# Performance work log

Hardware: AMD Instinct MI355X
Metric: run time of the kernel (lower is better)

The kernel has to match this reference:

```python
import jax, jax.numpy as jnp
import numpy as np

N_NODES = 100000
N_EDGES = 1600000


def gcn_conv(x, src, dst, W, b, n_nodes):
    # PyG GCNConv: h = x @ W; symmetric normalization with self-loops; scatter-add; + bias
    deg = jax.ops.segment_sum(jnp.ones_like(src, dtype=x.dtype), dst, num_segments=n_nodes)
    dinv = jax.lax.rsqrt(jnp.where(deg > 0, deg, 1.0))
    norm = dinv[src] * dinv[dst]              # [E+N]
    h = x @ W                                  # [N, out]
    msg = h[src] * norm[:, None]               # gather + scale (irregular access)
    out = jax.ops.segment_sum(msg, dst, num_segments=n_nodes)  # scatter-add aggregate
    return out + b


def setup_inputs() -> dict:
    key = jax.random.key(0)
    k1, k2, k3, k4 = jax.random.split(key, 4)
    x = jax.random.normal(k1, (N_NODES, 128), dtype=jnp.float32)
    edge_index = jax.random.randint(k2, (2, N_EDGES), 0, N_NODES, dtype=jnp.int64)
    W1 = jax.random.normal(k3, (128, 48), dtype=jnp.float32) * (1.0 / np.sqrt(128))
    b1 = jnp.zeros((48,), dtype=jnp.float32)
    W2 = jax.random.normal(k4, (48, 16), dtype=jnp.float32) * (1.0 / np.sqrt(48))
    b2 = jnp.zeros((16,), dtype=jnp.float32)
    return {"x": x, "edge_index": edge_index, "W1": W1, "b1": b1, "W2": W2, "b2": b2}


def reference(x, edge_index, W1, b1, W2, b2):
    n = x.shape[0]
    loops = jnp.arange(n, dtype=edge_index.dtype)
    src = jnp.concatenate([edge_index[0], loops])  # add self-loops
    dst = jnp.concatenate([edge_index[1], loops])
    h = gcn_conv(x, src, dst, W1, b1, n)
    h = jax.nn.relu(h)
    h = gcn_conv(h, src, dst, W2, b2, n)
    h = jax.nn.relu(h)
    return jax.nn.softmax(h, axis=1)
```

## Files before the change

### kernel.cpp

```cpp
#include <hip/hip_runtime.h>
#include <hip/hip_bf16.h>
#include <hip/hip_fp16.h>


#define TILE 4096

typedef _Float16 half8 __attribute__((ext_vector_type(8)));
typedef float floatx4 __attribute__((ext_vector_type(4)));

__global__ __launch_bounds__(256) void k_bhist(const int* __restrict__ dst, int E,
                                               int* __restrict__ Hw, int nbuck) {
    __shared__ int h[512];
    int t = threadIdx.x;
    for (int i = t; i < nbuck; i += 256) h[i] = 0;
    __syncthreads();
    int base = blockIdx.x * TILE;
#pragma unroll
    for (int r = 0; r < TILE / 256; ++r) {
        int e = base + r * 256 + t;
        if (e < E) atomicAdd(&h[dst[e] >> 8], 1);
    }
    __syncthreads();
    for (int i = t; i < nbuck; i += 256) Hw[blockIdx.x * nbuck + i] = h[i];
}

__global__ __launch_bounds__(256) void k_bsum(const int* __restrict__ Hw, int nTiles,
                                              int nbuck, int* __restrict__ btot) {
    int wid = (blockIdx.x * 256 + threadIdx.x) >> 6;
    int lane = threadIdx.x & 63;
    if (wid >= nbuck) return;
    int sum = 0;
    for (int tt = lane; tt < nTiles; tt += 64) sum += Hw[tt * nbuck + wid];
#pragma unroll
    for (int off = 32; off; off >>= 1) sum += __shfl_down(sum, off);
    if (lane == 0) btot[wid] = sum;
}

__global__ __launch_bounds__(512) void k_bscan2(const int* __restrict__ btot, int nbuck,
                                                int* __restrict__ bstart) {
    __shared__ int s[512];
    int t = threadIdx.x;
    int v = (t < nbuck) ? btot[t] : 0;
    s[t] = v;
    __syncthreads();
    for (int off = 1; off < 512; off <<= 1) {
        int tmp = (t >= off) ? s[t - off] : 0;
        __syncthreads();
        s[t] += tmp;
        __syncthreads();
    }
    if (t < nbuck) bstart[t] = s[t] - v;
    if (t == nbuck - 1) bstart[nbuck] = s[t];
}

__global__ __launch_bounds__(256) void k_boff(int* __restrict__ Hw, int nTiles,
                                              int nbuck, const int* __restrict__ bstart) {
    int wid = (blockIdx.x * 256 + threadIdx.x) >> 6;
    int lane = threadIdx.x & 63;
    if (wid >= nbuck) return;
    int running = bstart[wid];
    for (int chunk = 0; chunk < nTiles; chunk += 64) {
        int tt = chunk + lane;
        int v = (tt < nTiles) ? Hw[tt * nbuck + wid] : 0;
        int incl = v;
#pragma unroll
        for (int off = 1; off < 64; off <<= 1) {
            int u = __shfl_up(incl, off);
            if (lane >= off) incl += u;
        }
        if (tt < nTiles) Hw[tt * nbuck + wid] = running + (incl - v);
        running += __shfl(incl, 63);
    }
}

__global__ __launch_bounds__(256) void k_bscatter(const int* __restrict__ ei, int E,
                                                  const int* __restrict__ Hw, int nbuck,
                                                  int* __restrict__ ebuf) {
    __shared__ int cur[512];
    int t = threadIdx.x;
    for (int i = t; i < nbuck; i += 256) cur[i] = Hw[blockIdx.x * nbuck + i];
    __syncthreads();
    int base = blockIdx.x * TILE;
#pragma unroll
    for (int r = 0; r < TILE / 256; ++r) {
        int e = base + r * 256 + t;
        if (e < E) {
            int s = ei[e];
            int d = ei[E + e];
            int pos = atomicAdd(&cur[d >> 8], 1);
            ebuf[pos] = s | ((d & 255) << 17);
        }
    }
}

__global__ __launch_bounds__(256) void k_csrfill(const int* __restrict__ ebuf,
                                                 const int* __restrict__ bstart,
                                                 int* __restrict__ csr,
                                                 int* __restrict__ rowstart,
                                                 float* __restrict__ dinv, int N) {
    __shared__ int lcnt[256];
    __shared__ int lscan[256];
    __shared__ int lcur[256];
    int t = threadIdx.x;
    int nodebase = blockIdx.x << 8;
    int segs = bstart[blockIdx.x];
    int sege = bstart[blockIdx.x + 1];
    lcnt[t] = 0;
    __syncthreads();
    for (int i = segs + t; i < sege; i += 256)
        atomicAdd(&lcnt[((unsigned)ebuf[i]) >> 17], 1);
    __syncthreads();
    int v = lcnt[t];
    lscan[t] = v;
    __syncthreads();
    for (int off = 1; off < 256; off <<= 1) {
        int tmp = (t >= off) ? lscan[t - off] : 0;
        __syncthreads();
        lscan[t] += tmp;
        __syncthreads();
    }
    int excl = lscan[t] - v;
    int node = nodebase + t;
    int rs = segs + excl;
    if (node < N) {
        rowstart[node] = rs;
        dinv[node] = rsqrtf((float)(v + 1));
        if (node == N - 1) rowstart[N] = rs + v;
    }
    lcur[t] = rs;
    __syncthreads();
    for (int i = segs + t; i < sege; i += 256) {
        int pk = ebuf[i];
        int pos = atomicAdd(&lcur[((unsigned)pk) >> 17], 1);
        csr[pos] = pk & 0x1FFFF;
    }
}

__global__ __launch_bounds__(256) void k_gemm1(const float* __restrict__ x,
                                               const float* __restrict__ W1,
                                               const float* __restrict__ dinv,
                                               __half* __restrict__ h1p, int N) {
    __shared__ _Float16 wt[48 * 136];
    int t = threadIdx.x;
    for (int i = t; i < 128 * 48; i += 256) {
        int k = i / 48, c = i % 48;
        wt[c * 136 + k] = (_Float16)W1[i];
    }
    __syncthreads();

    int wave = t >> 6, lane = t & 63;
    int g = lane >> 4;
    int rtile = blockIdx.x * 64 + wave * 16;
    int rowA = rtile + (lane & 15);
    const float* xrow = x + (size_t)(rowA < N ? rowA : N - 1) * 128;
    int c0 = lane & 15;

    floatx4 acc[3];
#pragma unroll
    for (int nt = 0; nt < 3; ++nt)
#pragma unroll
        for (int q = 0; q < 4; ++q) acc[nt][q] = 0.f;

#pragma unroll
    for (int kc = 0; kc < 4; ++kc) {
        int k0 = kc * 32 + g * 8;
        float4 a0 = *(const float4*)(xrow + k0);
        float4 a1 = *(const float4*)(xrow + k0 + 4);
        half8 a;
        a[0] = (_Float16)a0.x; a[1] = (_Float16)a0.y;
        a[2] = (_Float16)a0.z; a[3] = (_Float16)a0.w;
        a[4] = (_Float16)a1.x; a[5] = (_Float16)a1.y;
        a[6] = (_Float16)a1.z; a[7] = (_Float16)a1.w;
#pragma unroll
        for (int nt = 0; nt < 3; ++nt) {
            half8 b = *(const half8*)(&wt[(nt * 16 + c0) * 136 + k0]);
            acc[nt] = __builtin_amdgcn_mfma_f32_16x16x32_f16(a, b, acc[nt], 0, 0, 0);
        }
    }

    int rbase = rtile + g * 4;
#pragma unroll
    for (int j = 0; j < 4; ++j) {
        int r = rbase + j;
        if (r < N) {
            float dr = dinv[r];
#pragma unroll
            for (int nt = 0; nt < 3; ++nt)
                h1p[(size_t)r * 48 + nt * 16 + c0] = __float2half(acc[nt][j] * dr);
        }
    }
}

__global__ __launch_bounds__(256) void k_agg1(const __half* __restrict__ h1p,
                                              const int* __restrict__ csr,
                                              const int* __restrict__ rowstart,
                                              const float* __restrict__ dinv,
                                              const float* __restrict__ b1,
                                              __half* __restrict__ r1h, int N) {
    int wave = threadIdx.x >> 6;
    int lane = threadIdx.x & 63;
    int v = blockIdx.x * 4 + wave;
    if (v >= N) return;
    int grp = lane >> 3;
    int sub = lane & 7;

    int start = rowstart[v];
    int d = rowstart[v + 1] - start;
    float dv = dinv[v];
    const int* cs = csr + start;
    const char* h1b = (const char*)h1p;

    float acc[8] = {0.f, 0.f, 0.f, 0.f, 0.f, 0.f, 0.f, 0.f};

    for (int base = 0; base < d; base += 64) {
        int sreg = (base + lane < d) ? cs[base + lane] : 0;
        int nb = min(64, d - base);
        for (int j = 0; j < 8 && j * 8 < nb; ++j) {
            int s = __shfl(sreg, j * 8 + grp);
            if (j * 8 + grp < nb && sub < 6) {
                float4 rv = *(const float4*)(h1b + (size_t)s * 96 + sub * 16);
                const __half2* hp = (const __half2*)&rv;
#pragma unroll
                for (int q = 0; q < 4; ++q) {
                    float2 f = __half22float2(hp[q]);
                    acc[q * 2] += f.x;
                    acc[q * 2 + 1] += f.y;
                }
            }
        }
    }
#pragma unroll
    for (int i = 0; i < 8; ++i) {
        acc[i] += __shfl_xor(acc[i], 8);
        acc[i] += __shfl_xor(acc[i], 16);
        acc[i] += __shfl_xor(acc[i], 32);
    }
    if (grp == 0 && sub < 6) {
        float4 sv = *(const float4*)(h1b + (size_t)v * 96 + sub * 16);
        const __half2* hp = (const __half2*)&sv;
        __half2 ob[4];
#pragma unroll
        for (int q = 0; q < 4; ++q) {
            float2 sf = __half22float2(hp[q]);
            int fi = sub * 8 + q * 2;
            float o0 = fmaxf(dv * (acc[q * 2] + sf.x) + b1[fi], 0.f);
            float o1 = fmaxf(dv * (acc[q * 2 + 1] + sf.y) + b1[fi + 1], 0.f);
            ob[q] = __floats2half2_rn(o0, o1);
        }
        *(float4*)((char*)r1h + (size_t)v * 96 + sub * 16) = *(const float4*)ob;
    }
}

__global__ __launch_bounds__(256) void k_gemm2(const __half* __restrict__ r1h,
                                               const float* __restrict__ W2,
                                               const float* __restrict__ dinv,
                                               __half* __restrict__ h2p, int N) {
    __shared__ float w2s[48 * 16];
    int t = threadIdx.x;
    for (int i = t; i < 768; i += 256) w2s[i] = W2[i];
    __syncthreads();
    int flat = blockIdx.x * 256 + t;
    int row = flat >> 2;
    int cg = (flat & 3) * 4;
    if (row >= N) return;
    float4 acc = make_float4(0.f, 0.f, 0.f, 0.f);
    const __half2* xr = (const __half2*)((const char*)r1h + (size_t)row * 96);
#pragma unroll 4
    for (int kk = 0; kk < 24; ++kk) {
        float2 a = __half22float2(xr[kk]);
        float4 b0 = *(const float4*)(w2s + (2 * kk) * 16 + cg);
        float4 b1v = *(const float4*)(w2s + (2 * kk + 1) * 16 + cg);
        acc.x += a.x * b0.x + a.y * b1v.x;
        acc.y += a.x * b0.y + a.y * b1v.y;
        acc.z += a.x * b0.z + a.y * b1v.z;
        acc.w += a.x * b0.w + a.y * b1v.w;
    }
    float dr = dinv[row];
    __half2 h01 = __floats2half2_rn(acc.x * dr, acc.y * dr);
    __half2 h23 = __floats2half2_rn(acc.z * dr, acc.w * dr);
    __half* dst = h2p + (size_t)row * 16 + cg;
    *(__half2*)(dst) = h01;
    *(__half2*)(dst + 2) = h23;
}

__global__ __launch_bounds__(256) void k_agg2(const __half* __restrict__ h2p,
                                              const int* __restrict__ csr,
                                              const int* __restrict__ rowstart,
                                              const float* __restrict__ dinv,
                                              const float* __restrict__ b2,
                                              float* __restrict__ out, int N) {
    int tid = threadIdx.x;
    int lane = tid & 63;
    int hf = lane >> 5;
    int l32 = lane & 31;
    int grp = l32 >> 1;
    int sub = lane & 1;
    int v = (blockIdx.x * 4 + (tid >> 6)) * 2 + hf;
    if (v >= N) return;

    int start = rowstart[v];
    int d = rowstart[v + 1] - start;
    float dv = dinv[v];
    const int* cs = csr + start;
    const char* h2b = (const char*)h2p;

    float acc[8] = {0.f, 0.f, 0.f, 0.f, 0.f, 0.f, 0.f, 0.f};

    for (int base = 0; base < d; base += 32) {
        int sreg = (base + l32 < d) ? cs[base + l32] : 0;
        int nb = min(32, d - base);
#pragma unroll
        for (int j = 0; j < 2; ++j) {
            int e = j * 16 + grp;
            int s = __shfl(sreg, (hf << 5) + e);
            if (e < nb) {
                float4 rv = *(const float4*)(h2b + (size_t)s * 32 + sub * 16);
                const __half2* hp = (const __half2*)&rv;
#pragma unroll
                for (int q = 0; q < 4; ++q) {
                    float2 f = __half22float2(hp[q]);
                    acc[q * 2] += f.x;
                    acc[q * 2 + 1] += f.y;
                }
            }
        }
    }
#pragma unroll
    for (int i = 0; i < 8; ++i) {
        acc[i] += __shfl_xor(acc[i], 2);
        acc[i] += __shfl_xor(acc[i], 4);
        acc[i] += __shfl_xor(acc[i], 8);
        acc[i] += __shfl_xor(acc[i], 16);
    }
    if (grp == 0) {
        float4 sv = *(const float4*)(h2b + (size_t)v * 32 + sub * 16);
        const __half2* hp = (const __half2*)&sv;
        float z[8];
#pragma unroll
        for (int q = 0; q < 4; ++q) {
            float2 f = __half22float2(hp[q]);
            z[q * 2]     = fmaxf(dv * (acc[q * 2] + f.x) + b2[sub * 8 + q * 2], 0.f);
            z[q * 2 + 1] = fmaxf(dv * (acc[q * 2 + 1] + f.y) + b2[sub * 8 + q * 2 + 1], 0.f);
        }
        float m8 = z[0];
#pragma unroll
        for (int i = 1; i < 8; ++i) m8 = fmaxf(m8, z[i]);
        float m = fmaxf(m8, __shfl_xor(m8, 1));
        float p[8];
        float s8 = 0.f;
#pragma unroll
        for (int i = 0; i < 8; ++i) { p[i] = __expf(z[i] - m); s8 += p[i]; }
        float inv = 1.f / (s8 + __shfl_xor(s8, 1));
        float4* dst = (float4*)(out + (size_t)v * 16 + sub * 8);
        dst[0] = make_float4(p[0] * inv, p[1] * inv, p[2] * inv, p[3] * inv);
        dst[1] = make_float4(p[4] * inv, p[5] * inv, p[6] * inv, p[7] * inv);
    }
}

extern "C" void kernel_launch(void* const* d_in, const int* in_sizes, int n_in,
                              void* d_out, int out_size, void* d_ws, size_t ws_size,
                              hipStream_t stream) {
    const float* x  = (const float*)d_in[0];
    const int*   ei = (const int*)d_in[1];
    const float* W1 = (const float*)d_in[2];
    const float* b1 = (const float*)d_in[3];
    const float* W2 = (const float*)d_in[4];
    const float* b2 = (const float*)d_in[5];
    float* out = (float*)d_out;

    int N = in_sizes[0] / 128;
    int E = in_sizes[1] / 2;
    int NBK = (N + 255) >> 8;
    int nTiles = (E + TILE - 1) / TILE;

    char* p = (char*)d_ws;
    auto alloc = [&](size_t bytes) -> char* {
        char* q = p;
        p += (bytes + 255) & ~(size_t)255;
        return q;
    };
    int*    rowstart = (int*)alloc((size_t)(N + 1) * 4);
    float*  dinv     = (float*)alloc((size_t)N * 4);
    int*    btot     = (int*)alloc((size_t)NBK * 4);
    int*    bstart   = (int*)alloc((size_t)(NBK + 1) * 4);
    int*    Hw       = (int*)alloc((size_t)nTiles * NBK * 4);
    int*    csr      = (int*)alloc((size_t)E * 4);
    size_t  ovl_sz   = (size_t)N * 48 * 2 > (size_t)E * 4 ? (size_t)N * 48 * 2
                                                          : (size_t)E * 4;
    char*   ovl      = alloc(ovl_sz);
    int*    ebuf     = (int*)ovl;
    __half* h1p      = (__half*)ovl;
    __half* r1h      = (__half*)alloc((size_t)N * 48 * 2);
    __half* h2p      = h1p;

    int wgBuck = (NBK + 3) / 4;

    hipLaunchKernelGGL(k_bhist, dim3(nTiles), dim3(256), 0, stream, ei + E, E, Hw, NBK);
    hipLaunchKernelGGL(k_bsum, dim3(wgBuck), dim3(256), 0, stream, Hw, nTiles, NBK, btot);
    hipLaunchKernelGGL(k_bscan2, dim3(1), dim3(512), 0, stream, btot, NBK, bstart);
    hipLaunchKernelGGL(k_boff, dim3(wgBuck), dim3(256), 0, stream, Hw, nTiles, NBK, bstart);
    hipLaunchKernelGGL(k_bscatter, dim3(nTiles), dim3(256), 0, stream, ei, E, Hw, NBK, ebuf);
    hipLaunchKernelGGL(k_csrfill, dim3(NBK), dim3(256), 0, stream,
                       ebuf, bstart, csr, rowstart, dinv, N);
    hipLaunchKernelGGL(k_gemm1, dim3((N + 63) / 64), dim3(256), 0, stream,
                       x, W1, dinv, h1p, N);
    hipLaunchKernelGGL(k_agg1, dim3((N + 3) / 4), dim3(256), 0, stream,
                       h1p, csr, rowstart, dinv, b1, r1h, N);
    hipLaunchKernelGGL(k_gemm2, dim3((N * 4 + 255) / 256), dim3(256), 0, stream,
                       r1h, W2, dinv, h2p, N);
    hipLaunchKernelGGL(k_agg2, dim3((N + 7) / 8), dim3(256), 0, stream,
                       h2p, csr, rowstart, dinv, b2, out, N);
}
```

Before: 143.7 us.

## Vectorize edge loads in CSR build and fold bucket scan into offset kernel

The histogram, scatter and CSR-fill kernels now read edge indices and packed entries as int4 vectors, with scalar handling for unaligned head and tail elements. The single-block bucket scan kernel is removed, and each wave in k_boff computes its own bucket prefix by summing btot directly, which saves one launch. The agg2 inner loop now exits early when the second half-chunk is empty. The redundant prefix sums add some work, and the int4 load in k_bhist assumes 16-byte alignment of dst.

```diff
diff --git a/kernel.cpp b/kernel.cpp
--- a/kernel.cpp
+++ b/kernel.cpp
@@ -16,9 +16,18 @@
     __syncthreads();
     int base = blockIdx.x * TILE;
 #pragma unroll
-    for (int r = 0; r < TILE / 256; ++r) {
-        int e = base + r * 256 + t;
-        if (e < E) atomicAdd(&h[dst[e] >> 8], 1);
+    for (int r = 0; r < TILE / 1024; ++r) {
+        int e = base + (r * 256 + t) * 4;
+        if (e + 3 < E) {
+            int4 d4 = *(const int4*)(dst + e);
+            atomicAdd(&h[d4.x >> 8], 1);
+            atomicAdd(&h[d4.y >> 8], 1);
+            atomicAdd(&h[d4.z >> 8], 1);
+            atomicAdd(&h[d4.w >> 8], 1);
+        } else {
+            for (int k = 0; k < 4; ++k)
+                if (e + k < E) atomicAdd(&h[dst[e + k] >> 8], 1);
+        }
     }
     __syncthreads();
     for (int i = t; i < nbuck; i += 256) Hw[blockIdx.x * nbuck + i] = h[i];
@@ -36,29 +45,22 @@
     if (lane == 0) btot[wid] = sum;
 }
 
-__global__ __launch_bounds__(512) void k_bscan2(const int* __restrict__ btot, int nbuck,
-                                                int* __restrict__ bstart) {
-    __shared__ int s[512];
-    int t = threadIdx.x;
-    int v = (t < nbuck) ? btot[t] : 0;
-    s[t] = v;
-    __syncthreads();
-    for (int off = 1; off < 512; off <<= 1) {
-        int tmp = (t >= off) ? s[t - off] : 0;
-        __syncthreads();
-        s[t] += tmp;
-        __syncthreads();
-    }
-    if (t < nbuck) bstart[t] = s[t] - v;
-    if (t == nbuck - 1) bstart[nbuck] = s[t];
-}
-
 __global__ __launch_bounds__(256) void k_boff(int* __restrict__ Hw, int nTiles,
-                                              int nbuck, const int* __restrict__ bstart) {
+                                              int nbuck, const int* __restrict__ btot,
+                                              int* __restrict__ bstart) {
     int wid = (blockIdx.x * 256 + threadIdx.x) >> 6;
     int lane = threadIdx.x & 63;
     if (wid >= nbuck) return;
-    int running = bstart[wid];
+    int ps = 0;
+    for (int j = lane; j < wid; j += 64) ps += btot[j];
+#pragma unroll
+    for (int off = 32; off; off >>= 1) ps += __shfl_down(ps, off);
+    int prefix = __shfl(ps, 0);
+    if (lane == 0) {
+        bstart[wid] = prefix;
+        if (wid == nbuck - 1) bstart[nbuck] = prefix + btot[wid];
+    }
+    int running = prefix;
     for (int chunk = 0; chunk < nTiles; chunk += 64) {
         int tt = chunk + lane;
         int v = (tt < nTiles) ? Hw[tt * nbuck + wid] : 0;
@@ -81,14 +83,31 @@
     for (int i = t; i < nbuck; i += 256) cur[i] = Hw[blockIdx.x * nbuck + i];
     __syncthreads();
     int base = blockIdx.x * TILE;
-#pragma unroll
-    for (int r = 0; r < TILE / 256; ++r) {
-        int e = base + r * 256 + t;
-        if (e < E) {
-            int s = ei[e];
-            int d = ei[E + e];
-            int pos = atomicAdd(&cur[d >> 8], 1);
-            ebuf[pos] = s | ((d & 255) << 17);
+    bool al = (E & 3) == 0;
+#pragma unroll
+    for (int r = 0; r < TILE / 1024; ++r) {
+        int e = base + (r * 256 + t) * 4;
+        if (al && e + 3 < E) {
+            int4 s4 = *(const int4*)(ei + e);
+            int4 d4 = *(const int4*)(ei + E + e);
+            int p0 = atomicAdd(&cur[d4.x >> 8], 1);
+            ebuf[p0] = s4.x | ((d4.x & 255) << 17);
+            int p1 = atomicAdd(&cur[d4.y >> 8], 1);
+            ebuf[p1] = s4.y | ((d4.y & 255) << 17);
+            int p2 = atomicAdd(&cur[d4.z >> 8], 1);
+            ebuf[p2] = s4.z | ((d4.z & 255) << 17);
+            int p3 = atomicAdd(&cur[d4.w >> 8], 1);
+            ebuf[p3] = s4.w | ((d4.w & 255) << 17);
+        } else {
+            for (int k = 0; k < 4; ++k) {
+                int ek = e + k;
+                if (ek < E) {
+                    int s = ei[ek];
+                    int d = ei[E + ek];
+                    int pos = atomicAdd(&cur[d >> 8], 1);
+                    ebuf[pos] = s | ((d & 255) << 17);
+                }
+            }
         }
     }
 }
@@ -105,9 +124,22 @@
     int nodebase = blockIdx.x << 8;
     int segs = bstart[blockIdx.x];
     int sege = bstart[blockIdx.x + 1];
+    int vstart = (segs + 3) & ~3;
+    if (vstart > sege) vstart = sege;
+    int vend = sege & ~3;
+    if (vend < vstart) vend = vstart;
     lcnt[t] = 0;
     __syncthreads();
-    for (int i = segs + t; i < sege; i += 256)
+    for (int i = segs + t; i < vstart; i += 256)
+        atomicAdd(&lcnt[((unsigned)ebuf[i]) >> 17], 1);
+    for (int i = vstart + t * 4; i < vend; i += 1024) {
+        int4 p4 = *(const int4*)(ebuf + i);
+        atomicAdd(&lcnt[((unsigned)p4.x) >> 17], 1);
+        atomicAdd(&lcnt[((unsigned)p4.y) >> 17], 1);
+        atomicAdd(&lcnt[((unsigned)p4.z) >> 17], 1);
+        atomicAdd(&lcnt[((unsigned)p4.w) >> 17], 1);
+    }
+    for (int i = vend + t; i < sege; i += 256)
         atomicAdd(&lcnt[((unsigned)ebuf[i]) >> 17], 1);
     __syncthreads();
     int v = lcnt[t];
@@ -129,7 +161,23 @@
     }
     lcur[t] = rs;
     __syncthreads();
-    for (int i = segs + t; i < sege; i += 256) {
+    for (int i = segs + t; i < vstart; i += 256) {
+        int pk = ebuf[i];
+        int pos = atomicAdd(&lcur[((unsigned)pk) >> 17], 1);
+        csr[pos] = pk & 0x1FFFF;
+    }
+    for (int i = vstart + t * 4; i < vend; i += 1024) {
+        int4 p4 = *(const int4*)(ebuf + i);
+        int pos0 = atomicAdd(&lcur[((unsigned)p4.x) >> 17], 1);
+        csr[pos0] = p4.x & 0x1FFFF;
+        int pos1 = atomicAdd(&lcur[((unsigned)p4.y) >> 17], 1);
+        csr[pos1] = p4.y & 0x1FFFF;
+        int pos2 = atomicAdd(&lcur[((unsigned)p4.z) >> 17], 1);
+        csr[pos2] = p4.z & 0x1FFFF;
+        int pos3 = atomicAdd(&lcur[((unsigned)p4.w) >> 17], 1);
+        csr[pos3] = p4.w & 0x1FFFF;
+    }
+    for (int i = vend + t; i < sege; i += 256) {
         int pk = ebuf[i];
         int pos = atomicAdd(&lcur[((unsigned)pk) >> 17], 1);
         csr[pos] = pk & 0x1FFFF;
@@ -309,8 +357,7 @@
     for (int base = 0; base < d; base += 32) {
         int sreg = (base + l32 < d) ? cs[base + l32] : 0;
         int nb = min(32, d - base);
-#pragma unroll
-        for (int j = 0; j < 2; ++j) {
+        for (int j = 0; j < 2 && j * 16 < nb; ++j) {
             int e = j * 16 + grp;
             int s = __shfl(sreg, (hf << 5) + e);
             if (e < nb) {
@@ -397,8 +444,8 @@
 
     hipLaunchKernelGGL(k_bhist, dim3(nTiles), dim3(256), 0, stream, ei + E, E, Hw, NBK);
     hipLaunchKernelGGL(k_bsum, dim3(wgBuck), dim3(256), 0, stream, Hw, nTiles, NBK, btot);
-    hipLaunchKernelGGL(k_bscan2, dim3(1), dim3(512), 0, stream, btot, NBK, bstart);
-    hipLaunchKernelGGL(k_boff, dim3(wgBuck), dim3(256), 0, stream, Hw, nTiles, NBK, bstart);
+    hipLaunchKernelGGL(k_boff, dim3(wgBuck), dim3(256), 0, stream, Hw, nTiles, NBK,
+                       btot, bstart);
     hipLaunchKernelGGL(k_bscatter, dim3(nTiles), dim3(256), 0, stream, ei, E, Hw, NBK, ebuf);
     hipLaunchKernelGGL(k_csrfill, dim3(NBK), dim3(256), 0, stream,
                        ebuf, bstart, csr, rowstart, dinv, N);
```

Result: faster. 137.8 us (-4.1%).
